# Kernel tuning notes

Measured on AMD Instinct MI355X. Metric: run time of the kernel, lower is better.

Reference implementation:

```python
import jax, jax.numpy as jnp
import numpy as np

NUM_TASKS = 150
ACT_DIM = 4
ENC_DIM = 256
EMB_DIM = 32
HEAD_HID = 128
B, H, W = 256, 128, 128


def _conv(x, w, b):
    # x: NCHW, w: OIHW, stride 2, padding 1 (torch Conv2d semantics)
    y = jax.lax.conv_general_dilated(x, w, window_strides=(2, 2),
                                     padding=((1, 1), (1, 1)),
                                     dimension_numbers=('NCHW', 'OIHW', 'NCHW'))
    return y + b[None, :, None, None]


def setup_inputs() -> dict:
    key = jax.random.key(0)
    ks = iter(jax.random.split(key, 32))
    s = 0.05
    d = {
        'images': jax.random.normal(next(ks), (B, 3, H, W), jnp.float32),
        'proprioception': jax.random.normal(next(ks), (B, 7), jnp.float32),
        'task_ids': jax.random.randint(next(ks), (B,), 0, NUM_TASKS, jnp.int32),
        # vision encoder convs (OIHW)
        'c1_w': jax.random.normal(next(ks), (64, 3, 3, 3), jnp.float32) * s,
        'c1_b': jnp.zeros((64,), jnp.float32),
        'c2_w': jax.random.normal(next(ks), (128, 64, 3, 3), jnp.float32) * s,
        'c2_b': jnp.zeros((128,), jnp.float32),
        'c3_w': jax.random.normal(next(ks), (256, 128, 3, 3), jnp.float32) * s,
        'c3_b': jnp.zeros((256,), jnp.float32),
        # proprioception encoder (weights stored as [in, out])
        'p1_w': jax.random.normal(next(ks), (7, 64), jnp.float32) * s,
        'p1_b': jnp.zeros((64,), jnp.float32),
        'p2_w': jax.random.normal(next(ks), (64, 64), jnp.float32) * s,
        'p2_b': jnp.zeros((64,), jnp.float32),
        # shared-encoder fusion MLP (320 -> 256 -> 256)
        'f1_w': jax.random.normal(next(ks), (256 + 64, ENC_DIM), jnp.float32) * s,
        'f1_b': jnp.zeros((ENC_DIM,), jnp.float32),
        'f2_w': jax.random.normal(next(ks), (ENC_DIM, ENC_DIM), jnp.float32) * s,
        'f2_b': jnp.zeros((ENC_DIM,), jnp.float32),
        # task embedding table
        'task_emb': jax.random.normal(next(ks), (NUM_TASKS, EMB_DIM), jnp.float32) * s,
        # policy-level fusion (288 -> 256), dropout is identity at inference
        'g_w': jax.random.normal(next(ks), (ENC_DIM + EMB_DIM, ENC_DIM), jnp.float32) * s,
        'g_b': jnp.zeros((ENC_DIM,), jnp.float32),
        # stacked task-specific heads [num_tasks, in, out]
        'h1_w': jax.random.normal(next(ks), (NUM_TASKS, ENC_DIM, HEAD_HID), jnp.float32) * s,
        'h1_b': jnp.zeros((NUM_TASKS, HEAD_HID), jnp.float32),
        'h2_w': jax.random.normal(next(ks), (NUM_TASKS, HEAD_HID, HEAD_HID), jnp.float32) * s,
        'h2_b': jnp.zeros((NUM_TASKS, HEAD_HID), jnp.float32),
        'h3_w': jax.random.normal(next(ks), (NUM_TASKS, HEAD_HID, ACT_DIM), jnp.float32) * s,
        'h3_b': jnp.zeros((NUM_TASKS, ACT_DIM), jnp.float32),
    }
    return d


def reference(images, proprioception, task_ids,
              c1_w, c1_b, c2_w, c2_b, c3_w, c3_b,
              p1_w, p1_b, p2_w, p2_b,
              f1_w, f1_b, f2_w, f2_b,
              task_emb, g_w, g_b,
              h1_w, h1_b, h2_w, h2_b, h3_w, h3_b):
    relu = jax.nn.relu
    # vision encoder: 3 strided convs + global avg pool (AdaptiveAvgPool2d(1,1))
    v = relu(_conv(images, c1_w, c1_b))
    v = relu(_conv(v, c2_w, c2_b))
    v = relu(_conv(v, c3_w, c3_b))
    v = jnp.mean(v, axis=(2, 3))                      # [B, 256]
    # proprioception encoder (no final ReLU)
    p = relu(proprioception @ p1_w + p1_b) @ p2_w + p2_b  # [B, 64]
    # shared fusion
    f = relu(jnp.concatenate([v, p], axis=1) @ f1_w + f1_b)
    f = relu(f @ f2_w + f2_b)                         # [B, 256]
    # task embedding + policy fusion (dropout = identity in eval)
    e = task_emb[task_ids]                            # [B, 32]
    z = relu(jnp.concatenate([f, e], axis=1) @ g_w + g_b)  # [B, 256]
    # routed task heads: gather per-sample expert params, batched matmuls
    a = relu(jnp.einsum('bd,bdh->bh', z, h1_w[task_ids]) + h1_b[task_ids])
    a = relu(jnp.einsum('bd,bdh->bh', a, h2_w[task_ids]) + h2_b[task_ids])
    a = jnp.einsum('bd,bdh->bh', a, h3_w[task_ids]) + h3_b[task_ids]  # [B, 4]
    return a
```

## Files before the change

kernel.cpp:

```cpp
#include <hip/hip_runtime.h>
#include <hip/hip_bf16.h>

#define DIV_UP(a,b) (((a)+(b)-1)/(b))

typedef __attribute__((ext_vector_type(8))) short short8;
typedef __attribute__((ext_vector_type(4))) float f32x4;

__device__ __forceinline__ ushort bf16_bits(float x) {
    return __builtin_bit_cast(ushort, __float2bfloat16(x));
}

__global__ __launch_bounds__(256) void halo_zero_kernel(
    uint4* __restrict__ act1, uint4* __restrict__ act2,
    float4* __restrict__ vbuf) {
    const int b = blockIdx.x, tid = threadIdx.x;
    const uint4 z = {0u, 0u, 0u, 0u};
    uint4* a1 = act1 + (size_t)b * 33800;
    for (int i = tid; i < 520; i += 256) a1[i] = z;
    for (int i = tid; i < 512; i += 256) {
        int r = (i >> 3) + 1;
        a1[r * 520 + (i & 7)] = z;
    }
    uint4* a2 = act2 + (size_t)b * 17424;
    for (int i = tid; i < 528; i += 256) a2[i] = z;
    for (int i = tid; i < 512; i += 256) {
        int r = (i >> 4) + 1;
        a2[r * 528 + (i & 15)] = z;
    }
    int idx = b * 256 + tid;
    float4 zf = {0.f, 0.f, 0.f, 0.f};
    if (idx < 16384) vbuf[idx] = zf;
}

__global__ void transpose_w1_kernel(const float* __restrict__ src,
                                    float* __restrict__ dst) {
    int t = blockIdx.x * blockDim.x + threadIdx.x;
    if (t >= 1728) return;
    int oc = t % 64;
    int r  = t / 64;
    int q  = r % 9;
    int c  = r / 9;
    dst[t] = src[(oc * 3 + c) * 9 + q];
}

__global__ void repack_w_kernel(const float* __restrict__ src,
                                __hip_bfloat16* __restrict__ dst, int O, int C) {
    int t = blockIdx.x * blockDim.x + threadIdx.x;
    if (t >= O * C * 9) return;
    int e   = t & 7;
    int r   = t >> 3;
    int n   = r % O;
    int q   = r / O;
    int SEG = C >> 3;
    int sg  = q % SEG;
    int tap = q / SEG;
    dst[t] = __float2bfloat16(src[(n * C + sg * 8 + e) * 9 + tap]);
}

__global__ __launch_bounds__(256) void conv1_kernel(
    const float* __restrict__ in, const float* __restrict__ wt ,
    const float* __restrict__ bias, __hip_bfloat16* __restrict__ out) {
    const int tid  = threadIdx.x;
    const int lane = tid & 63;
    const int wv   = tid >> 6;
    const int oh   = blockIdx.x;
    const int b    = blockIdx.y;

    __shared__ float  sx[3][3][132];
    __shared__ ushort sc[64][72];

    const float* ip  = in + (size_t)b * 3 * 128 * 128;
    const int    ih0 = 2 * oh - 1;
    for (int e = tid; e < 1170; e += 256) {
        int c   = e / 390;
        int rem = e - c * 390;
        int r   = rem / 130;
        int col = rem - r * 130;
        int ih  = ih0 + r;
        int iw  = col - 1;
        bool ok = ((unsigned)ih < 128u) && ((unsigned)iw < 128u);
        sx[c][r][col] = ok ? ip[c * 16384 + ih * 128 + iw] : 0.f;
    }
    __syncthreads();

    const int oc0 = __builtin_amdgcn_readfirstlane(wv << 4);
    const float* wts = wt + oc0;
    float acc[16];
#pragma unroll
    for (int i = 0; i < 16; ++i) acc[i] = bias[oc0 + i];
#pragma unroll
    for (int c = 0; c < 3; ++c)
#pragma unroll
        for (int kh = 0; kh < 3; ++kh)
#pragma unroll
            for (int kw = 0; kw < 3; ++kw) {
                float x = sx[c][kh][2 * lane + kw];
                const float* wrow = wts + (c * 9 + kh * 3 + kw) * 64;
#pragma unroll
                for (int i = 0; i < 16; ++i) acc[i] = fmaf(x, wrow[i], acc[i]);
            }

#pragma unroll
    for (int h = 0; h < 2; ++h) {
        union { uint4 u4; ushort s[8]; } pk;
#pragma unroll
        for (int e = 0; e < 8; ++e)
            pk.s[e] = bf16_bits(fmaxf(acc[h * 8 + e], 0.f));
        *(uint4*)&sc[lane][oc0 + h * 8] = pk.u4;
    }
    __syncthreads();

    __hip_bfloat16* obase = out + (((size_t)b * 65 + oh + 1) * 65 + 1) * 64;
#pragma unroll
    for (int s = 0; s < 2; ++s) {
        int g   = tid * 32 + s * 16;
        int pix = g >> 7;
        int col = (g & 127) >> 1;
        uint4 val = *(const uint4*)&sc[pix][col];
        *(uint4*)((char*)obase + g) = val;
    }
}

__global__ __launch_bounds__(256, 2) void conv2_gemm_kernel(
    const __hip_bfloat16* __restrict__ act,
    const __hip_bfloat16* __restrict__ wtB,
    const float* __restrict__ bias,
    __hip_bfloat16* __restrict__ out) {
    const int tid  = threadIdx.x;
    const int lane = tid & 63;
    const int w    = tid >> 6;
    const int l15  = lane & 15;
    const int quad = lane >> 4;
    const int per  = gridDim.x >> 3;
    const int Mt   = (blockIdx.x & 7) * per + (blockIdx.x >> 3);
    const int bimg = Mt >> 3;
    const int oh0  = (Mt & 7) << 2;

    __shared__ __align__(16) char smem[37504];
    ushort* As = (ushort*)smem;
    ushort* Cs = (ushort*)smem;

    f32x4 acc[4][4];
#pragma unroll
    for (int i = 0; i < 4; ++i)
#pragma unroll
        for (int j = 0; j < 4; ++j) acc[i][j] = (f32x4){0.f, 0.f, 0.f, 0.f};

    const int wm = (w & 1) << 6;
    const int wn = (w >> 1) << 6;
    const size_t abase = ((size_t)(bimg * 65 + 2 * oh0)) * 65 * 64;

    for (int h = 0; h < 2; ++h) {
        __syncthreads();
#pragma unroll
        for (int it = 0; it < 10; ++it) {
            int e = tid + (it << 8);
            if (e < 2340) {
                int s = e & 3, p = e >> 2;
                uint4 val = *(const uint4*)(act + abase + (size_t)p * 64 +
                                            h * 32 + s * 8);
                *(uint4*)(As + p * 32 + (((s ^ (p >> 1)) & 3) << 3)) = val;
            }
        }
        __syncthreads();
#pragma unroll
        for (int tap = 0; tap < 9; ++tap) {
            const int kh = tap / 3, kw = tap - kh * 3;
            short8 af[4], bf[4];
#pragma unroll
            for (int i = 0; i < 4; ++i) {
                int ml = wm + i * 16 + l15;
                int p  = ((ml >> 5) * 2 + kh) * 65 + ((ml & 31) * 2 + kw);
                af[i] = __builtin_bit_cast(short8,
                    *(const uint4*)(As + p * 32 + (((quad ^ (p >> 1)) & 3) << 3)));
            }
#pragma unroll
            for (int j = 0; j < 4; ++j)
                bf[j] = __builtin_bit_cast(short8,
                    *(const uint4*)(wtB +
                        ((size_t)((tap * 8 + h * 4 + quad) * 128) +
                         wn + j * 16 + l15) * 8));
#pragma unroll
            for (int i = 0; i < 4; ++i)
#pragma unroll
                for (int j = 0; j < 4; ++j)
                    acc[i][j] = __builtin_amdgcn_mfma_f32_16x16x32_bf16(
                        af[i], bf[j], acc[i][j], 0, 0, 0);
        }
    }

    __syncthreads();
#pragma unroll
    for (int j = 0; j < 4; ++j) {
        int n = wn + j * 16 + l15;
        float bv = bias[n];
#pragma unroll
        for (int i = 0; i < 4; ++i)
#pragma unroll
            for (int r = 0; r < 4; ++r) {
                int ml = wm + i * 16 + quad * 4 + r;
                Cs[ml * 132 + n] = bf16_bits(fmaxf(acc[i][j][r] + bv, 0.f));
            }
    }
    __syncthreads();
#pragma unroll
    for (int q = 0; q < 16; ++q) {
        int c   = tid + 256 * q;
        int row = c >> 5;
        int off = c & 31;
        uint2 val = *(const uint2*)(Cs + row * 132 + off * 4);
        int m  = (Mt << 7) + row;
        int b  = m >> 10;
        int rr = m & 1023;
        int oh = rr >> 5;
        int ow = rr & 31;
        size_t pix = ((size_t)(b * 33 + oh + 1) * 33 + (ow + 1));
        *(uint2*)(out + pix * 128 + off * 4) = val;
    }
}

__global__ __launch_bounds__(256, 2) void conv3_gemm_pool_kernel(
    const __hip_bfloat16* __restrict__ act,
    const __hip_bfloat16* __restrict__ wtB,
    const float* __restrict__ bias,
    float* __restrict__ v ) {
    const int tid  = threadIdx.x;
    const int lane = tid & 63;
    const int w    = tid >> 6;
    const int l15  = lane & 15;
    const int quad = lane >> 4;
    const int per  = gridDim.x >> 3;
    const int Mt   = (blockIdx.x & 7) * per + (blockIdx.x >> 3);
    const int bimg = Mt >> 2;
    const int oh0  = (Mt & 3) << 2;

    __shared__ __align__(16) char smem[38016];
    ushort* As   = (ushort*)smem;
    float*  sred = (float*)smem;

    f32x4 acc[4][4];
#pragma unroll
    for (int i = 0; i < 4; ++i)
#pragma unroll
        for (int j = 0; j < 4; ++j) acc[i][j] = (f32x4){0.f, 0.f, 0.f, 0.f};

    const int wn = w << 6;
    const size_t abase = ((size_t)(bimg * 33 + 2 * oh0)) * 33 * 128;

    for (int h = 0; h < 2; ++h) {
        __syncthreads();
#pragma unroll
        for (int it = 0; it < 10; ++it) {
            int e = tid + (it << 8);
            if (e < 2376) {
                int s = e & 7, p = e >> 3;
                uint4 val = *(const uint4*)(act + abase + (size_t)p * 128 +
                                            h * 64 + s * 8);
                *(uint4*)(As + p * 64 + (((s ^ (p >> 1)) & 7) << 3)) = val;
            }
        }
        __syncthreads();
#pragma unroll 1
        for (int tap = 0; tap < 9; ++tap) {
            const int kh = tap / 3, kw = tap - kh * 3;
#pragma unroll
            for (int ks = 0; ks < 2; ++ks) {
                short8 af[4], bf[4];
                const int sl = ks * 4 + quad;
#pragma unroll
                for (int i = 0; i < 4; ++i) {
                    int p = (i * 2 + kh) * 33 + l15 * 2 + kw;
                    af[i] = __builtin_bit_cast(short8,
                        *(const uint4*)(As + p * 64 +
                                        (((sl ^ (p >> 1)) & 7) << 3)));
                }
#pragma unroll
                for (int j = 0; j < 4; ++j)
                    bf[j] = __builtin_bit_cast(short8,
                        *(const uint4*)(wtB +
                            ((size_t)((tap * 16 + h * 8 + sl) * 256) +
                             wn + j * 16 + l15) * 8));
#pragma unroll
                for (int i = 0; i < 4; ++i)
#pragma unroll
                    for (int j = 0; j < 4; ++j)
                        acc[i][j] = __builtin_amdgcn_mfma_f32_16x16x32_bf16(
                            af[i], bf[j], acc[i][j], 0, 0, 0);
            }
        }
    }

    float s4[4];
#pragma unroll
    for (int j = 0; j < 4; ++j) {
        float bv = bias[wn + j * 16 + l15];
        float s = 0.f;
#pragma unroll
        for (int i = 0; i < 4; ++i)
#pragma unroll
            for (int r = 0; r < 4; ++r)
                s += fmaxf(acc[i][j][r] + bv, 0.f);
        s += __shfl_xor(s, 16, 64);
        s += __shfl_xor(s, 32, 64);
        s4[j] = s;
    }
    __syncthreads();
    if (quad == 0) {
#pragma unroll
        for (int j = 0; j < 4; ++j) sred[wn + j * 16 + l15] = s4[j];
    }
    __syncthreads();
    atomicAdd(v + (size_t)bimg * 256 + tid, sred[tid] * (1.f / 256.f));
}

template<int N, int K, int S, bool RELU>
__device__ __forceinline__ void gemv_stage(const float* __restrict__ w,
                                           const float* __restrict__ bias,
                                           const float* in, float* outv,
                                           float4* red4, int tid) {
    constexpr int G = N / 4;
    constexpr int CHK = K / S;
    static_assert(G * S == 256 && CHK * S == K, "stage shape");
    const int g = tid % G, s = tid / G;
    const float4* wp = (const float4*)w;
    float4 a; a.x = a.y = a.z = a.w = 0.f;
    const int k0 = s * CHK;
#pragma unroll 8
    for (int i = 0; i < CHK; ++i) {
        float x = in[k0 + i];
        float4 wv = wp[(size_t)(k0 + i) * G + g];
        a.x = fmaf(x, wv.x, a.x);
        a.y = fmaf(x, wv.y, a.y);
        a.z = fmaf(x, wv.z, a.z);
        a.w = fmaf(x, wv.w, a.w);
    }
    red4[tid] = a;
    __syncthreads();
    if (tid < N) {
        int gg = tid >> 2, e = tid & 3;
        float vv = bias[tid];
#pragma unroll
        for (int ss = 0; ss < S; ++ss) {
            const float* rp = (const float*)(red4 + ss * G + gg);
            vv += rp[e];
        }
        if (RELU) vv = fmaxf(vv, 0.f);
        outv[tid] = vv;
    }
    __syncthreads();
}

__global__ __launch_bounds__(256) void tail_kernel(
    const float* __restrict__ prop, const int* __restrict__ task_ids,
    const float* __restrict__ p1_w, const float* __restrict__ p1_b,
    const float* __restrict__ p2_w, const float* __restrict__ p2_b,
    const float* __restrict__ v,
    const float* __restrict__ f1_w, const float* __restrict__ f1_b,
    const float* __restrict__ f2_w, const float* __restrict__ f2_b,
    const float* __restrict__ task_emb,
    const float* __restrict__ g_w, const float* __restrict__ g_b,
    const float* __restrict__ h1_w, const float* __restrict__ h1_b,
    const float* __restrict__ h2_w, const float* __restrict__ h2_b,
    const float* __restrict__ h3_w, const float* __restrict__ h3_b,
    float* __restrict__ out) {
    const int b   = blockIdx.x;
    const int tid = threadIdx.x;
    const int t   = task_ids[b];
    __shared__ float sa[320];
    __shared__ float sb[288];
    __shared__ float sph[64];
    __shared__ float4 red4[256];

    sa[tid] = (tid < 256) ? v[(size_t)b * 256 + tid] : 0.f;
    if (tid < 64) {
        float h = p1_b[tid];
#pragma unroll
        for (int k = 0; k < 7; ++k) h = fmaf(prop[b * 7 + k], p1_w[k * 64 + tid], h);
        sph[tid] = fmaxf(h, 0.f);
    }
    __syncthreads();
    gemv_stage<64, 64, 16, false>(p2_w, p2_b, sph, sa + 256, red4, tid);
    gemv_stage<256, 320, 4, true>(f1_w, f1_b, sa, sb, red4, tid);
    gemv_stage<256, 256, 4, true>(f2_w, f2_b, sb, sa, red4, tid);
    if (tid < 32) sa[256 + tid] = task_emb[t * 32 + tid];
    __syncthreads();
    gemv_stage<256, 288, 4, true>(g_w, g_b, sa, sb, red4, tid);
    gemv_stage<128, 256, 8, true>(h1_w + (size_t)t * 32768, h1_b + t * 128,
                                  sb, sa, red4, tid);
    gemv_stage<128, 128, 8, true>(h2_w + (size_t)t * 16384, h2_b + t * 128,
                                  sa, sb, red4, tid);
    if (tid < 128) {
        float4 wv = ((const float4*)(h3_w + (size_t)t * 512))[tid];
        float x = sb[tid];
        float r0 = x * wv.x, r1 = x * wv.y, r2 = x * wv.z, r3 = x * wv.w;
#pragma unroll
        for (int off = 1; off < 64; off <<= 1) {
            r0 += __shfl_xor(r0, off, 64);
            r1 += __shfl_xor(r1, off, 64);
            r2 += __shfl_xor(r2, off, 64);
            r3 += __shfl_xor(r3, off, 64);
        }
        if ((tid & 63) == 0) {
            float4 rv; rv.x = r0; rv.y = r1; rv.z = r2; rv.w = r3;
            red4[tid >> 6] = rv;
        }
    }
    __syncthreads();
    if (tid < 4) {
        const float* ra = (const float*)(red4 + 0);
        const float* rb = (const float*)(red4 + 1);
        out[b * 4 + tid] = ra[tid] + rb[tid] + h3_b[t * 4 + tid];
    }
}

extern "C" void kernel_launch(void* const* d_in, const int* in_sizes, int n_in,
                              void* d_out, int out_size, void* d_ws, size_t ws_size,
                              hipStream_t stream) {
    (void)in_sizes; (void)n_in; (void)out_size;
    const float* images   = (const float*)d_in[0];
    const float* prop     = (const float*)d_in[1];
    const int*   task_ids = (const int*)d_in[2];
    const float* c1_w = (const float*)d_in[3];
    const float* c1_b = (const float*)d_in[4];
    const float* c2_w = (const float*)d_in[5];
    const float* c2_b = (const float*)d_in[6];
    const float* c3_w = (const float*)d_in[7];
    const float* c3_b = (const float*)d_in[8];
    const float* p1_w = (const float*)d_in[9];
    const float* p1_b = (const float*)d_in[10];
    const float* p2_w = (const float*)d_in[11];
    const float* p2_b = (const float*)d_in[12];
    const float* f1_w = (const float*)d_in[13];
    const float* f1_b = (const float*)d_in[14];
    const float* f2_w = (const float*)d_in[15];
    const float* f2_b = (const float*)d_in[16];
    const float* temb = (const float*)d_in[17];
    const float* g_w  = (const float*)d_in[18];
    const float* g_b  = (const float*)d_in[19];
    const float* h1_w = (const float*)d_in[20];
    const float* h1_b = (const float*)d_in[21];
    const float* h2_w = (const float*)d_in[22];
    const float* h2_b = (const float*)d_in[23];
    const float* h3_w = (const float*)d_in[24];
    const float* h3_b = (const float*)d_in[25];
    float* out = (float*)d_out;

    const size_t per_img = (size_t)65 * 65 * 64 * 2 + (size_t)33 * 33 * 128 * 2;
    const size_t fixed   = (size_t)256 * 256 * 4 + 1728 * 4 +
                           (size_t)73728 * 2 + (size_t)294912 * 2 + 4096;
    int CHI = 64;
    if (ws_size >= fixed + per_img * 256) CHI = 256;
    else if (ws_size >= fixed + per_img * 128) CHI = 128;

    char* ws = (char*)d_ws;
    size_t off = 0;
    auto alloc = [&](size_t bytes) {
        void* p = ws + off;
        off += (bytes + 255) & ~(size_t)255;
        return p;
    };
    __hip_bfloat16* act1 = (__hip_bfloat16*)alloc((size_t)CHI * 65 * 65 * 64 * 2);
    __hip_bfloat16* act2 = (__hip_bfloat16*)alloc((size_t)CHI * 33 * 33 * 128 * 2);
    float*          vbuf = (float*)alloc((size_t)256 * 256 * 4);
    float*          w1t  = (float*)alloc((size_t)1728 * 4);
    __hip_bfloat16* w2t  = (__hip_bfloat16*)alloc((size_t)73728 * 2);
    __hip_bfloat16* w3t  = (__hip_bfloat16*)alloc((size_t)294912 * 2);

    halo_zero_kernel<<<dim3(CHI), 256, 0, stream>>>(
        (uint4*)act1, (uint4*)act2, (float4*)vbuf);
    transpose_w1_kernel<<<DIV_UP(1728, 256), 256, 0, stream>>>(c1_w, w1t);
    repack_w_kernel<<<DIV_UP(73728, 256), 256, 0, stream>>>(c2_w, w2t, 128, 64);
    repack_w_kernel<<<DIV_UP(294912, 256), 256, 0, stream>>>(c3_w, w3t, 256, 128);

    for (int c0 = 0; c0 < 256; c0 += CHI) {
        const float* img_c = images + (size_t)c0 * 3 * 128 * 128;
        conv1_kernel<<<dim3(64, CHI), dim3(256), 0, stream>>>(
            img_c, w1t, c1_b, act1);
        conv2_gemm_kernel<<<dim3(CHI * 8), 256, 0, stream>>>(
            act1, w2t, c2_b, act2);
        conv3_gemm_pool_kernel<<<dim3(CHI * 4), 256, 0, stream>>>(
            act2, w3t, c3_b, vbuf + (size_t)c0 * 256);
    }
    tail_kernel<<<256, 256, 0, stream>>>(prop, task_ids, p1_w, p1_b, p2_w, p2_b,
                                         vbuf, f1_w, f1_b, f2_w, f2_b, temb,
                                         g_w, g_b, h1_w, h1_b, h2_w, h2_b,
                                         h3_w, h3_b, out);
}
```

Measured before the change: 375.2 us.

## Rewrite conv1 as bf16 MFMA GEMM with im2col in LDS over four-row tiles

Replaces the scalar FMA first convolution with an MFMA-based implicit GEMM. Each block now handles four output rows (256 pixels), builds a swizzled bf16 im2col tile with K padded from 27 to 32 in shared memory, and issues 16x16x32 bf16 MFMAs against bf16-repacked weights. The aim is to cut the FP32 FMA cost and the redundant weight loads of conv1 and to amortize the image staging over more rows. In exchange, inputs are rounded to bf16 before the multiply, and the kernel uses more shared memory and extra sync steps.

```diff
diff --git a/kernel.cpp b/kernel.cpp
--- a/kernel.cpp
+++ b/kernel.cpp
@@ -32,15 +32,14 @@
     if (idx < 16384) vbuf[idx] = zf;
 }
 
-__global__ void transpose_w1_kernel(const float* __restrict__ src,
-                                    float* __restrict__ dst) {
+__global__ void repack_w1_kernel(const float* __restrict__ src,
+                                 __hip_bfloat16* __restrict__ dst) {
     int t = blockIdx.x * blockDim.x + threadIdx.x;
-    if (t >= 1728) return;
-    int oc = t % 64;
-    int r  = t / 64;
-    int q  = r % 9;
-    int c  = r / 9;
-    dst[t] = src[(oc * 3 + c) * 9 + q];
+    if (t >= 2048) return;
+    int k  = t & 31;
+    int oc = t >> 5;
+    dst[t] = (k < 27) ? __float2bfloat16(src[oc * 27 + k])
+                      : __float2bfloat16(0.f);
 }
 
 __global__ void repack_w_kernel(const float* __restrict__ src,
@@ -57,67 +56,104 @@
     dst[t] = __float2bfloat16(src[(n * C + sg * 8 + e) * 9 + tap]);
 }
 
-__global__ __launch_bounds__(256) void conv1_kernel(
-    const float* __restrict__ in, const float* __restrict__ wt ,
-    const float* __restrict__ bias, __hip_bfloat16* __restrict__ out) {
+__global__ __launch_bounds__(256) void conv1_mfma_kernel(
+    const float* __restrict__ in,
+    const __hip_bfloat16* __restrict__ wB,
+    const float* __restrict__ bias,
+    __hip_bfloat16* __restrict__ out) {
     const int tid  = threadIdx.x;
     const int lane = tid & 63;
     const int wv   = tid >> 6;
-    const int oh   = blockIdx.x;
+    const int l15  = lane & 15;
+    const int quad = lane >> 4;
+    const int tile = blockIdx.x;
     const int b    = blockIdx.y;
-
-    __shared__ float  sx[3][3][132];
-    __shared__ ushort sc[64][72];
+    const int oh0  = tile << 2;
+
+    __shared__ __align__(16) char smem[36864];
+    float*  sx = (float*)smem;
+    ushort* Al = (ushort*)(smem + 14256);
+    ushort* Cs = (ushort*)smem;
 
     const float* ip  = in + (size_t)b * 3 * 128 * 128;
-    const int    ih0 = 2 * oh - 1;
-    for (int e = tid; e < 1170; e += 256) {
-        int c   = e / 390;
-        int rem = e - c * 390;
+    const int    ih0 = 2 * oh0 - 1;
+    for (int e = tid; e < 3510; e += 256) {
+        int c   = e / 1170;
+        int rem = e - c * 1170;
         int r   = rem / 130;
         int col = rem - r * 130;
         int ih  = ih0 + r;
         int iw  = col - 1;
         bool ok = ((unsigned)ih < 128u) && ((unsigned)iw < 128u);
-        sx[c][r][col] = ok ? ip[c * 16384 + ih * 128 + iw] : 0.f;
-    }
-    __syncthreads();
-
-    const int oc0 = __builtin_amdgcn_readfirstlane(wv << 4);
-    const float* wts = wt + oc0;
-    float acc[16];
-#pragma unroll
-    for (int i = 0; i < 16; ++i) acc[i] = bias[oc0 + i];
-#pragma unroll
-    for (int c = 0; c < 3; ++c)
-#pragma unroll
-        for (int kh = 0; kh < 3; ++kh)
-#pragma unroll
-            for (int kw = 0; kw < 3; ++kw) {
-                float x = sx[c][kh][2 * lane + kw];
-                const float* wrow = wts + (c * 9 + kh * 3 + kw) * 64;
-#pragma unroll
-                for (int i = 0; i < 16; ++i) acc[i] = fmaf(x, wrow[i], acc[i]);
-            }
-
-#pragma unroll
-    for (int h = 0; h < 2; ++h) {
-        union { uint4 u4; ushort s[8]; } pk;
-#pragma unroll
-        for (int e = 0; e < 8; ++e)
-            pk.s[e] = bf16_bits(fmaxf(acc[h * 8 + e], 0.f));
-        *(uint4*)&sc[lane][oc0 + h * 8] = pk.u4;
-    }
-    __syncthreads();
-
-    __hip_bfloat16* obase = out + (((size_t)b * 65 + oh + 1) * 65 + 1) * 64;
-#pragma unroll
-    for (int s = 0; s < 2; ++s) {
-        int g   = tid * 32 + s * 16;
-        int pix = g >> 7;
-        int col = (g & 127) >> 1;
-        uint4 val = *(const uint4*)&sc[pix][col];
-        *(uint4*)((char*)obase + g) = val;
+        sx[(c * 9 + r) * 132 + col] = ok ? ip[c * 16384 + ih * 128 + iw] : 0.f;
+    }
+    __syncthreads();
+
+    {
+        const int px = tid, ohl = px >> 6, ow = px & 63;
+        union { uint4 u4[4]; ushort us[32]; } rowv;
+#pragma unroll
+        for (int k = 0; k < 27; ++k) {
+            const int c = k / 9, rm = k - c * 9, kh = rm / 3, kw = rm - kh * 3;
+            rowv.us[k] = bf16_bits(sx[(c * 9 + 2 * ohl + kh) * 132 + 2 * ow + kw]);
+        }
+#pragma unroll
+        for (int k = 27; k < 32; ++k) rowv.us[k] = 0;
+#pragma unroll
+        for (int q = 0; q < 4; ++q)
+            *(uint4*)(Al + px * 32 + (((q ^ (px >> 1)) & 3) << 3)) = rowv.u4[q];
+    }
+    __syncthreads();
+
+    short8 af[4], bf[4];
+#pragma unroll
+    for (int i = 0; i < 4; ++i)
+        af[i] = __builtin_bit_cast(short8,
+            *(const uint4*)(wB + ((i * 16 + l15) * 32 + quad * 8)));
+#pragma unroll
+    for (int j = 0; j < 4; ++j) {
+        int p = wv * 64 + j * 16 + l15;
+        bf[j] = __builtin_bit_cast(short8,
+            *(const uint4*)(Al + p * 32 + (((quad ^ (p >> 1)) & 3) << 3)));
+    }
+    f32x4 acc[4][4];
+#pragma unroll
+    for (int i = 0; i < 4; ++i)
+#pragma unroll
+        for (int j = 0; j < 4; ++j)
+            acc[i][j] = __builtin_amdgcn_mfma_f32_16x16x32_bf16(
+                af[i], bf[j], (f32x4){0.f, 0.f, 0.f, 0.f}, 0, 0, 0);
+
+    float4 bv[4];
+#pragma unroll
+    for (int i = 0; i < 4; ++i)
+        bv[i] = *(const float4*)(bias + i * 16 + quad * 4);
+
+    __syncthreads();
+
+#pragma unroll
+    for (int j = 0; j < 4; ++j) {
+        const int px = wv * 64 + j * 16 + l15;
+#pragma unroll
+        for (int i = 0; i < 4; ++i) {
+            union { uint2 u2; ushort us[4]; } pk;
+#pragma unroll
+            for (int r = 0; r < 4; ++r)
+                pk.us[r] = bf16_bits(
+                    fmaxf(acc[i][j][r] + ((const float*)&bv[i])[r], 0.f));
+            *(uint2*)(Cs + px * 72 + i * 16 + quad * 4) = pk.u2;
+        }
+    }
+    __syncthreads();
+
+    __hip_bfloat16* ob = out + (((size_t)b * 65 + oh0 + 1) * 65 + 1) * 64;
+#pragma unroll
+    for (int it = 0; it < 8; ++it) {
+        int g   = it * 256 + tid;
+        int px  = g >> 3, cq = g & 7;
+        uint4 v = *(const uint4*)(Cs + px * 72 + cq * 8);
+        int ohl = px >> 6, ow = px & 63;
+        *(uint4*)(ob + ((size_t)ohl * 65 + ow) * 64 + cq * 8) = v;
     }
 }
 
@@ -462,20 +498,20 @@
     __hip_bfloat16* act1 = (__hip_bfloat16*)alloc((size_t)CHI * 65 * 65 * 64 * 2);
     __hip_bfloat16* act2 = (__hip_bfloat16*)alloc((size_t)CHI * 33 * 33 * 128 * 2);
     float*          vbuf = (float*)alloc((size_t)256 * 256 * 4);
-    float*          w1t  = (float*)alloc((size_t)1728 * 4);
+    __hip_bfloat16* w1b  = (__hip_bfloat16*)alloc((size_t)2048 * 2);
     __hip_bfloat16* w2t  = (__hip_bfloat16*)alloc((size_t)73728 * 2);
     __hip_bfloat16* w3t  = (__hip_bfloat16*)alloc((size_t)294912 * 2);
 
     halo_zero_kernel<<<dim3(CHI), 256, 0, stream>>>(
         (uint4*)act1, (uint4*)act2, (float4*)vbuf);
-    transpose_w1_kernel<<<DIV_UP(1728, 256), 256, 0, stream>>>(c1_w, w1t);
+    repack_w1_kernel<<<8, 256, 0, stream>>>(c1_w, w1b);
     repack_w_kernel<<<DIV_UP(73728, 256), 256, 0, stream>>>(c2_w, w2t, 128, 64);
     repack_w_kernel<<<DIV_UP(294912, 256), 256, 0, stream>>>(c3_w, w3t, 256, 128);
 
     for (int c0 = 0; c0 < 256; c0 += CHI) {
         const float* img_c = images + (size_t)c0 * 3 * 128 * 128;
-        conv1_kernel<<<dim3(64, CHI), dim3(256), 0, stream>>>(
-            img_c, w1t, c1_b, act1);
+        conv1_mfma_kernel<<<dim3(16, CHI), dim3(256), 0, stream>>>(
+            img_c, w1b, c1_b, act1);
         conv2_gemm_kernel<<<dim3(CHI * 8), 256, 0, stream>>>(
             act1, w2t, c2_b, act2);
         conv3_gemm_pool_kernel<<<dim3(CHI * 4), 256, 0, stream>>>(
```

Result: faster. 367.1 us (-2.2%).
